# Optimization experiments

Hardware: AMD Instinct MI355X
Metric: run time of the kernel (lower is better)

The kernel has to match this reference:

```python
import jax, jax.numpy as jnp
import numpy as np


def setup_inputs() -> dict:
    key = jax.random.key(0)
    ks = jax.random.split(key, 6)
    bs, T, F, HS, da, r = 64, 512, 128, 256, 64, 8
    s = 0.05  # xavier-ish scale, keeps gates out of saturation
    return {
        "x": jax.random.normal(ks[0], (bs, T, F), jnp.float32),
        "w_first": jax.random.normal(ks[1], (da, F), jnp.float32) * s,
        "b_first": jnp.zeros((da,), jnp.float32),
        "w_second": jax.random.normal(ks[2], (r, da), jnp.float32) * s,
        "b_second": jnp.zeros((r,), jnp.float32),
        "weight_iBarh": jax.random.normal(ks[3], (F, 4 * HS), jnp.float32) * s,
        "weight_hh": jax.random.normal(ks[4], (HS, 4 * HS), jnp.float32) * s,
        "bias": jnp.zeros((4 * HS,), jnp.float32),
    }


def reference(x, w_first, b_first, w_second, b_second, weight_iBarh, weight_hh, bias):
    bs, T, F = x.shape
    HS = weight_hh.shape[0]
    r = w_second.shape[0]
    # attention scores are a fixed per-position function of x -> precompute once
    scores = jnp.tanh(x @ w_first.T + b_first) @ w_second.T + b_second  # [bs, T, r]
    neg = jnp.finfo(x.dtype).min
    t_idx = jnp.arange(T)

    def step(carry, t):
        h, c = carry
        # growing-window softmax over time axis: positions 0..t
        mask = (t_idx <= t)[None, :, None]  # [1, T, 1]
        attn = jax.nn.softmax(jnp.where(mask, scores, neg), axis=1)  # [bs, T, r]
        # matrixM: attention^T @ pastTimeSteps, summed over r heads / r
        M = jnp.einsum('btr,btf->bf', attn, x) / r  # [bs, F]
        gates = M @ weight_iBarh + h @ weight_hh + bias  # [bs, 4*HS]
        i = jax.nn.sigmoid(gates[:, :HS])
        f = jax.nn.sigmoid(gates[:, HS:2 * HS])
        g = jnp.tanh(gates[:, 2 * HS:3 * HS])
        o = jax.nn.sigmoid(gates[:, 3 * HS:])
        c = f * c + i * g
        h = o * jnp.tanh(c)
        return (h, c), h

    h0 = jnp.zeros((bs, HS), x.dtype)
    c0 = jnp.zeros((bs, HS), x.dtype)
    (h_t, c_t), hs = jax.lax.scan(step, (h0, c0), t_idx)
    hidden_seq = jnp.transpose(hs, (1, 0, 2))  # [bs, T, HS]
    # attention returned by the torch code is from the LAST step (full window)
    attention = jnp.transpose(jax.nn.softmax(scores, axis=1), (0, 2, 1))  # [bs, r, T]
    return hidden_seq, h_t, c_t, attention
```

## Files before the change

### kernel.cpp

```cpp
#include <hip/hip_runtime.h>
#include <cmath>

#define T_LEN 512
#define BS    64
#define F_DIM 128
#define HSZ   256
#define DA    64
#define RH    8
#define KTOT  384

#define OFF_HT   8388608
#define OFF_CT   8404992
#define OFF_ATT  8421376

__global__ __launch_bounds__(256) void k_scores(
    const float* __restrict__ x, const float* __restrict__ w1,
    const float* __restrict__ b1, const float* __restrict__ w2,
    const float* __restrict__ b2, float* __restrict__ scores)
{
  __shared__ float wl[DA * 129];
  __shared__ float xs[4][F_DIM];
  __shared__ float hid[4][DA];
  int tid = threadIdx.x;
  for (int id = tid; id < DA * F_DIM; id += 256) {
    int a = id >> 7, f = id & 127;
    wl[a * 129 + f] = w1[id];
  }
  int wv = tid >> 6, lane = tid & 63;
  int pair = blockIdx.x * 4 + wv;
  const float* xr = x + (size_t)pair * F_DIM;
  xs[wv][lane]      = xr[lane];
  xs[wv][64 + lane] = xr[64 + lane];
  __syncthreads();
  float acc = b1[lane];
  #pragma unroll 8
  for (int f = 0; f < F_DIM; ++f)
    acc += xs[wv][f] * wl[lane * 129 + f];
  hid[wv][lane] = tanhf(acc);
  __syncthreads();
  if (lane < RH) {
    float sc = b2[lane];
    #pragma unroll 8
    for (int a = 0; a < DA; ++a)
      sc += hid[wv][a] * w2[lane * DA + a];
    scores[(size_t)pair * RH + lane] = sc;
  }
}

__global__ __launch_bounds__(512) void k_attn_M(
    const float* __restrict__ x, const float* __restrict__ scores,
    float* __restrict__ M, float* __restrict__ out)
{
  __shared__ float se[T_LEN * 9];
  __shared__ float ivd[T_LEN * 9];
  __shared__ float cp[4 * F_DIM * RH];
  __shared__ float gmax[RH];
  int tid = threadIdx.x;
  int b = blockIdx.x;
  const float* sb = scores + (size_t)b * T_LEN * RH;
  for (int id = tid; id < T_LEN * RH; id += 512)
    se[(id >> 3) * 9 + (id & 7)] = sb[id];
  __syncthreads();
  {
    int w = tid >> 6, l = tid & 63;
    float m = -INFINITY;
    #pragma unroll
    for (int i = 0; i < 8; ++i)
      m = fmaxf(m, se[(i * 64 + l) * 9 + w]);
    #pragma unroll
    for (int off = 32; off; off >>= 1)
      m = fmaxf(m, __shfl_xor(m, off));
    if (l == 0) gmax[w] = m;
  }
  __syncthreads();
  for (int id = tid; id < T_LEN * RH; id += 512) {
    int t = id >> 3, r = id & 7;
    se[t * 9 + r] = expf(se[t * 9 + r] - gmax[r]);
  }
  __syncthreads();
  if (tid < RH) {
    float run = 0.f;
    for (int t = 0; t < T_LEN; ++t) {
      run += se[t * 9 + tid];
      ivd[t * 9 + tid] = run;
    }
  }
  __syncthreads();
  for (int id = tid; id < T_LEN * RH; id += 512) {
    int t = id >> 3, r = id & 7;
    ivd[t * 9 + r] = 1.f / ivd[t * 9 + r];
  }
  __syncthreads();
  for (int id = tid; id < T_LEN * RH; id += 512) {
    int r = id >> 9, t = id & 511;
    out[OFF_ATT + ((size_t)b * RH + r) * T_LEN + t] = se[t * 9 + r] * ivd[511 * 9 + r];
  }
  int j = tid >> 7, f = tid & 127;
  const float* xb = x + (size_t)b * T_LEN * F_DIM;
  float part[RH];
  #pragma unroll
  for (int r = 0; r < RH; ++r) part[r] = 0.f;
  for (int t = j * 128; t < j * 128 + 128; ++t) {
    float xv = xb[t * F_DIM + f];
    #pragma unroll
    for (int r = 0; r < RH; ++r) part[r] += se[t * 9 + r] * xv;
  }
  {
    float* c = &cp[(j * F_DIM + f) * RH];
    #pragma unroll
    for (int r = 0; r < RH; ++r) c[r] = part[r];
  }
  __syncthreads();
  float num[RH];
  #pragma unroll
  for (int r = 0; r < RH; ++r) num[r] = 0.f;
  for (int jj = 0; jj < j; ++jj) {
    const float* c = &cp[(jj * F_DIM + f) * RH];
    #pragma unroll
    for (int r = 0; r < RH; ++r) num[r] += c[r];
  }
  float* Mb = M + (size_t)b * T_LEN * F_DIM;
  for (int t = j * 128; t < j * 128 + 128; ++t) {
    float xv = xb[t * F_DIM + f];
    float acc = 0.f;
    #pragma unroll
    for (int r = 0; r < RH; ++r) {
      num[r] += se[t * 9 + r] * xv;
      acc += num[r] * ivd[t * 9 + r];
    }
    Mb[t * F_DIM + f] = 0.125f * acc;
  }
}

__global__ __launch_bounds__(512, 2) void k_lstm(
    const float* __restrict__ M, const float* __restrict__ Wi,
    const float* __restrict__ Wh, const float* __restrict__ bias,
    unsigned long long* __restrict__ slab64,
    float* __restrict__ out)
{
  __shared__ float v[HSZ];
  __shared__ float mst[F_DIM];
  __shared__ float part[512];
  int tid = threadIdx.x;
  int blk = blockIdx.x;
  int s = blk >> 6;
  int b = blk & 63;
  int half = tid >> 8;
  int ct = tid & 255;
  int type = ct >> 6, j = ct & 63;
  int col = type * 256 + s * 64 + j;

  float w[192];
  {
    int k0 = half * 192;
    #pragma unroll
    for (int k = 0; k < 192; ++k) {
      int kk = k0 + k;
      w[k] = (kk < F_DIM) ? Wi[(size_t)kk * 1024 + col]
                          : Wh[(size_t)(kk - F_DIM) * 1024 + col];
    }
  }
  float bsum = bias[col];
  float c_reg = 0.f;

  if (tid < HSZ) v[tid] = 0.f;
  if (tid < F_DIM) mst[tid] = M[((size_t)b * T_LEN) * F_DIM + tid];
  __syncthreads();

  int pidx = tid >> 6;
  int sp = pidx + (pidx >= s);
  int pj = tid & 63;

  for (int t = 0; t < T_LEN; ++t) {
    float acc;
    if (half == 0) {
      acc = bsum;
      #pragma unroll
      for (int k = 0; k < 128; ++k) acc += mst[k] * w[k];
      #pragma unroll
      for (int k = 128; k < 192; ++k) acc += v[k - 128] * w[k];
    } else {
      acc = 0.f;
      #pragma unroll
      for (int k = 0; k < 192; ++k) acc += v[64 + k] * w[k];
    }
    part[tid] = acc;
    __syncthreads();

    if (tid < 64) {
      float gi = part[tid]       + part[256 + tid];
      float gf = part[64 + tid]  + part[320 + tid];
      float gg = part[128 + tid] + part[384 + tid];
      float go = part[192 + tid] + part[448 + tid];
      float ii = 1.f / (1.f + expf(-gi));
      float ff = 1.f / (1.f + expf(-gf));
      float gt = tanhf(gg);
      float oo = 1.f / (1.f + expf(-go));
      c_reg = ff * c_reg + ii * gt;
      float h = oo * tanhf(c_reg);
      int hsx = s * 64 + tid;
      v[hsx] = h;
      unsigned long long pk =
          ((unsigned long long)(unsigned)(t + 1) << 32) |
          (unsigned long long)__float_as_uint(h);
      __hip_atomic_store(&slab64[(((t & 1) * BS + b) * 4 + s) * 64 + tid], pk,
                         __ATOMIC_RELAXED, __HIP_MEMORY_SCOPE_AGENT);
      out[((size_t)b * T_LEN + t) * HSZ + hsx] = h;
      if (t == T_LEN - 1) {
        out[OFF_HT + b * HSZ + hsx] = h;
        out[OFF_CT + b * HSZ + hsx] = c_reg;
      }
    }

    if (t < T_LEN - 1) {
      float mreg = 0.f;
      if (tid < F_DIM)
        mreg = M[((size_t)b * T_LEN + t + 1) * F_DIM + tid];
      if (tid < 192) {
        const unsigned long long* addr =
            &slab64[(((t & 1) * BS + b) * 4 + sp) * 64 + pj];
        unsigned want = (unsigned)(t + 1);
        unsigned long long got;
        do {
          got = __hip_atomic_load(addr, __ATOMIC_RELAXED,
                                  __HIP_MEMORY_SCOPE_AGENT);
        } while ((unsigned)(got >> 32) != want);
        v[sp * 64 + pj] = __uint_as_float((unsigned)(got & 0xffffffffu));
      }
      if (tid < F_DIM) mst[tid] = mreg;
      __syncthreads();
    }
  }
}

extern "C" void kernel_launch(void* const* d_in, const int* in_sizes, int n_in,
                              void* d_out, int out_size, void* d_ws, size_t ws_size,
                              hipStream_t stream) {
  const float* x   = (const float*)d_in[0];
  const float* w1  = (const float*)d_in[1];
  const float* b1  = (const float*)d_in[2];
  const float* w2  = (const float*)d_in[3];
  const float* b2  = (const float*)d_in[4];
  const float* Wi  = (const float*)d_in[5];
  const float* Wh  = (const float*)d_in[6];
  const float* bia = (const float*)d_in[7];
  float* out = (float*)d_out;
  float* ws  = (float*)d_ws;

  float* scores = ws;
  float* M      = ws + 262144;
  unsigned long long* slab64 =
      (unsigned long long*)(ws + 262144 + 4194304);

  hipLaunchKernelGGL(k_scores, dim3(8192), dim3(256), 0, stream,
                     x, w1, b1, w2, b2, scores);
  hipLaunchKernelGGL(k_attn_M, dim3(64), dim3(512), 0, stream,
                     x, scores, M, out);
  hipLaunchKernelGGL(k_lstm, dim3(256), dim3(512), 0, stream,
                     M, Wi, Wh, bia, slab64, out);
}
```

Baseline: 1.196 ms.

## Split attention-M across time chunks and hoist input projection off LSTM critical path

k_attn_M now launches 4x more blocks, each handling one 128-step time chunk. Each block recomputes the prefix of scores and x it needs and replaces the serial per-head cumulative sum with a segmented parallel scan. In k_lstm, the M·Wi contribution for step t+1 is computed directly from global memory with float4 loads while the block waits on the inter-block spin. This removes 64 of the 192 serial shared-memory FMAs from each step's critical path. The cost is redundant prefix work in the attention blocks and uncoalesced per-thread M reads, which are likely L2 hits.

```diff
diff --git a/kernel.cpp b/kernel.cpp
--- a/kernel.cpp
+++ b/kernel.cpp
@@ -7,7 +7,6 @@
 #define HSZ   256
 #define DA    64
 #define RH    8
-#define KTOT  384
 
 #define OFF_HT   8388608
 #define OFF_CT   8404992
@@ -53,82 +52,110 @@
 {
   __shared__ float se[T_LEN * 9];
   __shared__ float ivd[T_LEN * 9];
+  __shared__ float segsum[RH][65];
   __shared__ float cp[4 * F_DIM * RH];
   __shared__ float gmax[RH];
   int tid = threadIdx.x;
-  int b = blockIdx.x;
+  int blk = blockIdx.x;
+  int j = blk >> 6, b = blk & 63;
+  int p0 = j * 128, e = p0 + 128;
+  int e8 = e * 8;
   const float* sb = scores + (size_t)b * T_LEN * RH;
-  for (int id = tid; id < T_LEN * RH; id += 512)
+  for (int id = tid; id < e8; id += 512)
     se[(id >> 3) * 9 + (id & 7)] = sb[id];
   __syncthreads();
   {
     int w = tid >> 6, l = tid & 63;
     float m = -INFINITY;
-    #pragma unroll
-    for (int i = 0; i < 8; ++i)
-      m = fmaxf(m, se[(i * 64 + l) * 9 + w]);
+    for (int t = l; t < e; t += 64)
+      m = fmaxf(m, se[t * 9 + w]);
     #pragma unroll
     for (int off = 32; off; off >>= 1)
       m = fmaxf(m, __shfl_xor(m, off));
     if (l == 0) gmax[w] = m;
   }
   __syncthreads();
-  for (int id = tid; id < T_LEN * RH; id += 512) {
+  for (int id = tid; id < e8; id += 512) {
     int t = id >> 3, r = id & 7;
     se[t * 9 + r] = expf(se[t * 9 + r] - gmax[r]);
   }
   __syncthreads();
+  int nseg = e >> 3;
+  {
+    int r = tid >> 6, seg = tid & 63;
+    if (seg < nseg) {
+      float run = 0.f;
+      #pragma unroll
+      for (int i = 0; i < 8; ++i) {
+        int t = seg * 8 + i;
+        run += se[t * 9 + r];
+        ivd[t * 9 + r] = run;
+      }
+      segsum[r][seg] = run;
+    }
+  }
+  __syncthreads();
   if (tid < RH) {
-    float run = 0.f;
-    for (int t = 0; t < T_LEN; ++t) {
-      run += se[t * 9 + tid];
-      ivd[t * 9 + tid] = run;
-    }
-  }
-  __syncthreads();
-  for (int id = tid; id < T_LEN * RH; id += 512) {
+    float off = 0.f;
+    for (int sg = 0; sg < nseg; ++sg) {
+      float tmp = segsum[tid][sg];
+      segsum[tid][sg] = off;
+      off += tmp;
+    }
+  }
+  __syncthreads();
+  for (int id = tid; id < e8; id += 512) {
     int t = id >> 3, r = id & 7;
-    ivd[t * 9 + r] = 1.f / ivd[t * 9 + r];
-  }
-  __syncthreads();
-  for (int id = tid; id < T_LEN * RH; id += 512) {
-    int r = id >> 9, t = id & 511;
-    out[OFF_ATT + ((size_t)b * RH + r) * T_LEN + t] = se[t * 9 + r] * ivd[511 * 9 + r];
-  }
-  int j = tid >> 7, f = tid & 127;
+    ivd[t * 9 + r] = 1.f / (ivd[t * 9 + r] + segsum[r][t >> 3]);
+  }
+  __syncthreads();
+  if (j == 3) {
+    for (int id = tid; id < T_LEN * RH; id += 512) {
+      int r = id >> 9, t = id & 511;
+      out[OFF_ATT + ((size_t)b * RH + r) * T_LEN + t] =
+          se[t * 9 + r] * ivd[511 * 9 + r];
+    }
+  }
   const float* xb = x + (size_t)b * T_LEN * F_DIM;
-  float part[RH];
-  #pragma unroll
-  for (int r = 0; r < RH; ++r) part[r] = 0.f;
-  for (int t = j * 128; t < j * 128 + 128; ++t) {
-    float xv = xb[t * F_DIM + f];
-    #pragma unroll
-    for (int r = 0; r < RH; ++r) part[r] += se[t * 9 + r] * xv;
-  }
-  {
-    float* c = &cp[(j * F_DIM + f) * RH];
-    #pragma unroll
-    for (int r = 0; r < RH; ++r) c[r] = part[r];
-  }
-  __syncthreads();
-  float num[RH];
-  #pragma unroll
-  for (int r = 0; r < RH; ++r) num[r] = 0.f;
-  for (int jj = 0; jj < j; ++jj) {
-    const float* c = &cp[(jj * F_DIM + f) * RH];
-    #pragma unroll
-    for (int r = 0; r < RH; ++r) num[r] += c[r];
-  }
-  float* Mb = M + (size_t)b * T_LEN * F_DIM;
-  for (int t = j * 128; t < j * 128 + 128; ++t) {
-    float xv = xb[t * F_DIM + f];
-    float acc = 0.f;
-    #pragma unroll
-    for (int r = 0; r < RH; ++r) {
-      num[r] += se[t * 9 + r] * xv;
-      acc += num[r] * ivd[t * 9 + r];
-    }
-    Mb[t * F_DIM + f] = 0.125f * acc;
+  {
+    int q = tid >> 7, f = tid & 127;
+    int len = p0 >> 2;
+    int t0 = q * len, t1 = t0 + len;
+    float pp[RH];
+    #pragma unroll
+    for (int r = 0; r < RH; ++r) pp[r] = 0.f;
+    for (int t = t0; t < t1; ++t) {
+      float xv = xb[t * F_DIM + f];
+      #pragma unroll
+      for (int r = 0; r < RH; ++r) pp[r] += se[t * 9 + r] * xv;
+    }
+    float* c = &cp[(q * F_DIM + f) * RH];
+    #pragma unroll
+    for (int r = 0; r < RH; ++r) c[r] = pp[r];
+  }
+  __syncthreads();
+  if (tid < F_DIM) {
+    int f = tid;
+    float num[RH];
+    #pragma unroll
+    for (int r = 0; r < RH; ++r) num[r] = 0.f;
+    #pragma unroll
+    for (int q = 0; q < 4; ++q) {
+      const float* c = &cp[(q * F_DIM + f) * RH];
+      #pragma unroll
+      for (int r = 0; r < RH; ++r) num[r] += c[r];
+    }
+    float* Mb = M + (size_t)b * T_LEN * F_DIM;
+    for (int t = p0; t < e; ++t) {
+      float xv = xb[t * F_DIM + f];
+      float acc = 0.f;
+      #pragma unroll
+      for (int r = 0; r < RH; ++r) {
+        num[r] += se[t * 9 + r] * xv;
+        acc += num[r] * ivd[t * 9 + r];
+      }
+      Mb[t * F_DIM + f] = 0.125f * acc;
+    }
   }
 }
 
@@ -139,7 +166,6 @@
     float* __restrict__ out)
 {
   __shared__ float v[HSZ];
-  __shared__ float mst[F_DIM];
   __shared__ float part[512];
   int tid = threadIdx.x;
   int blk = blockIdx.x;
@@ -147,43 +173,42 @@
   int b = blk & 63;
   int half = tid >> 8;
   int ct = tid & 255;
-  int type = ct >> 6, j = ct & 63;
-  int col = type * 256 + s * 64 + j;
-
-  float w[192];
-  {
-    int k0 = half * 192;
-    #pragma unroll
-    for (int k = 0; k < 192; ++k) {
-      int kk = k0 + k;
-      w[k] = (kk < F_DIM) ? Wi[(size_t)kk * 1024 + col]
-                          : Wh[(size_t)(kk - F_DIM) * 1024 + col];
-    }
-  }
-  float bsum = bias[col];
+  int type = ct >> 6, jj = ct & 63;
+  int col = type * 256 + s * 64 + jj;
+
+  float wm[64], wh[128];
+  #pragma unroll
+  for (int k = 0; k < 64; ++k)
+    wm[k] = Wi[(size_t)(half * 64 + k) * 1024 + col];
+  #pragma unroll
+  for (int k = 0; k < 128; ++k)
+    wh[k] = Wh[(size_t)(half * 128 + k) * 1024 + col];
+  float bsum = half ? 0.f : bias[col];
   float c_reg = 0.f;
 
   if (tid < HSZ) v[tid] = 0.f;
-  if (tid < F_DIM) mst[tid] = M[((size_t)b * T_LEN) * F_DIM + tid];
+
+  float macc = bsum;
+  {
+    const float4* mp = (const float4*)(M + (size_t)b * T_LEN * F_DIM + half * 64);
+    #pragma unroll
+    for (int k4 = 0; k4 < 16; ++k4) {
+      float4 m4 = mp[k4];
+      macc += m4.x * wm[4*k4] + m4.y * wm[4*k4+1]
+            + m4.z * wm[4*k4+2] + m4.w * wm[4*k4+3];
+    }
+  }
   __syncthreads();
 
   int pidx = tid >> 6;
   int sp = pidx + (pidx >= s);
   int pj = tid & 63;
+  int hoff = half * 128;
 
   for (int t = 0; t < T_LEN; ++t) {
-    float acc;
-    if (half == 0) {
-      acc = bsum;
-      #pragma unroll
-      for (int k = 0; k < 128; ++k) acc += mst[k] * w[k];
-      #pragma unroll
-      for (int k = 128; k < 192; ++k) acc += v[k - 128] * w[k];
-    } else {
-      acc = 0.f;
-      #pragma unroll
-      for (int k = 0; k < 192; ++k) acc += v[64 + k] * w[k];
-    }
+    float acc = macc;
+    #pragma unroll
+    for (int k = 0; k < 128; ++k) acc += v[hoff + k] * wh[k];
     part[tid] = acc;
     __syncthreads();
 
@@ -213,9 +238,18 @@
     }
 
     if (t < T_LEN - 1) {
-      float mreg = 0.f;
-      if (tid < F_DIM)
-        mreg = M[((size_t)b * T_LEN + t + 1) * F_DIM + tid];
+      {
+        const float4* mp =
+            (const float4*)(M + ((size_t)b * T_LEN + t + 1) * F_DIM + half * 64);
+        float nm = bsum;
+        #pragma unroll
+        for (int k4 = 0; k4 < 16; ++k4) {
+          float4 m4 = mp[k4];
+          nm += m4.x * wm[4*k4] + m4.y * wm[4*k4+1]
+              + m4.z * wm[4*k4+2] + m4.w * wm[4*k4+3];
+        }
+        macc = nm;
+      }
       if (tid < 192) {
         const unsigned long long* addr =
             &slab64[(((t & 1) * BS + b) * 4 + sp) * 64 + pj];
@@ -227,7 +261,6 @@
         } while ((unsigned)(got >> 32) != want);
         v[sp * 64 + pj] = __uint_as_float((unsigned)(got & 0xffffffffu));
       }
-      if (tid < F_DIM) mst[tid] = mreg;
       __syncthreads();
     }
   }
@@ -254,7 +287,7 @@
 
   hipLaunchKernelGGL(k_scores, dim3(8192), dim3(256), 0, stream,
                      x, w1, b1, w2, b2, scores);
-  hipLaunchKernelGGL(k_attn_M, dim3(64), dim3(512), 0, stream,
+  hipLaunchKernelGGL(k_attn_M, dim3(256), dim3(512), 0, stream,
                      x, scores, M, out);
   hipLaunchKernelGGL(k_lstm, dim3(256), dim3(512), 0, stream,
                      M, Wi, Wh, bia, slab64, out);
```

Result: slower. 1.951 ms (+63.1%).
